# Kernel optimization log

Hardware: AMD Instinct MI355X
Metric: run time of the kernel (lower is better)

## Reference

```python
import jax, jax.numpy as jnp
import numpy as np


def setup_inputs() -> dict:
    key = jax.random.key(0)
    ks = jax.random.split(key, 6)
    B, S, F = 8, 2048, 1024
    scale = 1.0 / np.sqrt(F)
    return {
        "query": jax.random.normal(ks[0], (B, S, F), dtype=jnp.float32),
        "key": jax.random.normal(ks[1], (B, S, F), dtype=jnp.float32),
        "value": jax.random.normal(ks[2], (B, S, F), dtype=jnp.float32),
        "Wq": jax.random.normal(ks[3], (F, F), dtype=jnp.float32) * scale,
        "Wk": jax.random.normal(ks[4], (F, F), dtype=jnp.float32) * scale,
        "Wv": jax.random.normal(ks[5], (F, F), dtype=jnp.float32) * scale,
    }


def reference(query, key, value, Wq, Wk, Wv):
    # nn.Linear(bias=False): x @ W.T, W is [out, in]
    q_t = jnp.einsum('bsf,gf->bsg', query, Wq)
    k_t = jnp.einsum('bsf,gf->bsg', key, Wk)
    v_t = jnp.einsum('bsf,gf->bsg', value, Wv)
    F = k_t.shape[-1]
    scale = jnp.asarray(1.0, q_t.dtype) / jnp.sqrt(jnp.asarray(F, q_t.dtype))
    attn = jnp.einsum('bij,bkj->bik', q_t, k_t) * scale  # [B, S, S]
    # original uses nn.Softmax(dim=1): softmax over the query (i) axis
    attn = jax.nn.softmax(attn, axis=1)
    # 'bii,bij->bij': diagonal of attn scales rows of v_t
    diag = jnp.diagonal(attn, axis1=1, axis2=2)  # [B, S]
    proj = diag[:, :, None] * v_t  # [B, S, F]
    return proj
```

## Files before the change

### kernel.cpp

```cpp
#include <hip/hip_runtime.h>


typedef _Float16 f16x8 __attribute__((ext_vector_type(8)));
typedef float    f32x4 __attribute__((ext_vector_type(4)));

#define COLIC 8
#define SCALE 0.03125f

typedef __attribute__((address_space(1))) const unsigned int g_u32_t;
typedef __attribute__((address_space(3))) unsigned int l_u32_t;

__device__ __forceinline__ void gload16(const _Float16* g, _Float16* l) {
  __builtin_amdgcn_global_load_lds((g_u32_t*)g, (l_u32_t*)l, 16, 0, 0);
}

__device__ __forceinline__ void stage_tile(const _Float16* gbase, int ldk,
                                           _Float16* lds, int w, int lane) {
#pragma unroll
  for (int c = 0; c < 2; ++c) {
    const int blk = c * 4 + w;
    const int r = (blk << 4) + (lane >> 2);
    const _Float16* g = gbase + (size_t)r * ldk + ((lane & 3) << 3);
    gload16(g, lds + blk * 512);
  }
}

__device__ __forceinline__ void stage_tile64(const _Float16* gbase, int ldk,
                                             _Float16* lds, int w, int lane) {
#pragma unroll
  for (int c = 0; c < 4; ++c) {
    const int blk = c * 4 + w;
    const int o = (blk << 10) + (lane << 4);
    const int row = o >> 7;
    const int colb = (o & 127) ^ ((row & 7) << 4);
    gload16(gbase + (size_t)row * ldk + (colb >> 1), lds + (blk << 9));
  }
}

struct Conv3Args {
  const float* src[3];
  _Float16* dst[3];
};
__global__ __launch_bounds__(256)
void conv3_f32_f16(Conv3Args a, int n8) {
  const float* __restrict__ src = a.src[blockIdx.y];
  _Float16* __restrict__ dst = a.dst[blockIdx.y];
  for (int i = blockIdx.x * 256 + threadIdx.x; i < n8; i += gridDim.x * 256) {
    const float4 x = ((const float4*)src)[2 * i];
    const float4 y = ((const float4*)src)[2 * i + 1];
    f16x8 o;
    o[0] = (_Float16)x.x; o[1] = (_Float16)x.y;
    o[2] = (_Float16)x.z; o[3] = (_Float16)x.w;
    o[4] = (_Float16)y.x; o[5] = (_Float16)y.y;
    o[6] = (_Float16)y.z; o[7] = (_Float16)y.w;
    ((f16x8*)dst)[i] = o;
  }
}

template <int F16OUT>
__global__ __launch_bounds__(256)
void gemm_mfma(const float* __restrict__ Af, const _Float16* __restrict__ Bh,
               _Float16* __restrict__ C16, float* __restrict__ C32,
               const float* __restrict__ mpart, const float* __restrict__ lpart,
               const float* __restrict__ sdiag, int BSz,
               int M, int N, int Kd) {
  __shared__ __align__(16) _Float16 As[128 * 32];
  __shared__ __align__(16) _Float16 Bs[128 * 32];
  __shared__ float diagS[128];
  const int tid = threadIdx.x;
  const int w = tid >> 6, lane = tid & 63;
  const int wr = w >> 1, wc = w & 1;
  const int lr = lane & 15, kq = lane >> 4;
  const int bm = blockIdx.x * 128, bn = blockIdx.y * 128;

  if (!F16OUT && tid < 128) {
    const int row = bm + tid;
    float Mx = -3.0e38f;
#pragma unroll
    for (int c = 0; c < COLIC; ++c) Mx = fmaxf(Mx, mpart[(size_t)c * BSz + row]);
    float L = 0.0f;
#pragma unroll
    for (int c = 0; c < COLIC; ++c)
      L += lpart[(size_t)c * BSz + row] * __expf(mpart[(size_t)c * BSz + row] - Mx);
    diagS[tid] = __expf(sdiag[row] - Mx) / L;
  }

  const int ar = lane >> 2;
  const int ac = (lane & 3) << 3;
  float4 pa[2][2];
#pragma unroll
  for (int c = 0; c < 2; ++c) {
    const int row = bm + (c * 4 + w) * 16 + ar;
    const float4* p = (const float4*)(Af + (size_t)row * Kd + ac);
    pa[c][0] = p[0]; pa[c][1] = p[1];
  }

  f32x4 acc[4][4] = {};
  for (int k0 = 0; k0 < Kd; k0 += 32) {
#pragma unroll
    for (int c = 0; c < 2; ++c) {
      const int blk = c * 4 + w;
      f16x8 v;
      v[0] = (_Float16)pa[c][0].x; v[1] = (_Float16)pa[c][0].y;
      v[2] = (_Float16)pa[c][0].z; v[3] = (_Float16)pa[c][0].w;
      v[4] = (_Float16)pa[c][1].x; v[5] = (_Float16)pa[c][1].y;
      v[6] = (_Float16)pa[c][1].z; v[7] = (_Float16)pa[c][1].w;
      *(f16x8*)&As[blk * 512 + lane * 8] = v;
    }
    stage_tile(Bh + (size_t)bn * Kd + k0, Kd, Bs, w, lane);
    const int kn = (k0 + 32 < Kd) ? k0 + 32 : 0;
#pragma unroll
    for (int c = 0; c < 2; ++c) {
      const int row = bm + (c * 4 + w) * 16 + ar;
      const float4* p = (const float4*)(Af + (size_t)row * Kd + kn + ac);
      pa[c][0] = p[0]; pa[c][1] = p[1];
    }
    __syncthreads();
    f16x8 af[4], bf[4];
#pragma unroll
    for (int mi = 0; mi < 4; ++mi)
      af[mi] = *(const f16x8*)&As[(wr * 64 + mi * 16 + lr) * 32 + kq * 8];
#pragma unroll
    for (int ni = 0; ni < 4; ++ni)
      bf[ni] = *(const f16x8*)&Bs[(wc * 64 + ni * 16 + lr) * 32 + kq * 8];
#pragma unroll
    for (int mi = 0; mi < 4; ++mi)
#pragma unroll
      for (int ni = 0; ni < 4; ++ni)
        acc[mi][ni] = __builtin_amdgcn_mfma_f32_16x16x32_f16(af[mi], bf[ni], acc[mi][ni], 0, 0, 0);
    __syncthreads();
  }
#pragma unroll
  for (int mi = 0; mi < 4; ++mi) {
#pragma unroll
    for (int j = 0; j < 4; ++j) {
      const int rloc = wr * 64 + mi * 16 + kq * 4 + j;
      const int row = bm + rloc;
      float s = 1.0f;
      if (!F16OUT) s = diagS[rloc];
#pragma unroll
      for (int ni = 0; ni < 4; ++ni) {
        const int col = bn + wc * 64 + ni * 16 + lr;
        if (F16OUT) C16[(size_t)row * N + col] = (_Float16)acc[mi][ni][j];
        else        C32[(size_t)row * N + col] = acc[mi][ni][j] * s;
      }
    }
  }
}

__global__ __launch_bounds__(256)
void col_stats_mfma(const _Float16* __restrict__ qt, const _Float16* __restrict__ kt,
                    float* __restrict__ mpart, float* __restrict__ lpart,
                    float* __restrict__ sdiag, int S, int Fd, int chunk) {
  __shared__ __align__(16) _Float16 Qs[128 * 64];
  __shared__ __align__(16) _Float16 Ks[128 * 64];
  __shared__ float redM[8][128];
  __shared__ float redL[8][128];
  const int b = blockIdx.z, jb = blockIdx.x, ic = blockIdx.y;
  const int j0 = jb * 128;
  const _Float16* Q = qt + (size_t)b * S * Fd;
  const _Float16* K = kt + (size_t)b * S * Fd;
  const int tid = threadIdx.x;
  const int w = tid >> 6, lane = tid & 63;
  const int wr = w >> 1, wc = w & 1;
  const int lr = lane & 15, kq = lane >> 4;
  const int swz = (lr & 7) << 4;

  float m[4], l[4];
#pragma unroll
  for (int ni = 0; ni < 4; ++ni) { m[ni] = -3.0e38f; l[ni] = 0.0f; }

  for (int it = 0; it < chunk >> 7; ++it) {
    const int i0 = ic * chunk + (it << 7);
    f32x4 acc[4][4] = {};
    for (int k0 = 0; k0 < Fd; k0 += 64) {
      stage_tile64(Q + (size_t)i0 * Fd + k0, Fd, Qs, w, lane);
      stage_tile64(K + (size_t)j0 * Fd + k0, Fd, Ks, w, lane);
      __syncthreads();
      f16x8 af[4][2], bf[4][2];
#pragma unroll
      for (int mi = 0; mi < 4; ++mi) {
        const int ro = (wr * 64 + mi * 16 + lr) << 7;
        af[mi][0] = *(const f16x8*)&Qs[(ro + ((kq * 16) ^ swz)) >> 1];
        af[mi][1] = *(const f16x8*)&Qs[(ro + ((64 + kq * 16) ^ swz)) >> 1];
      }
#pragma unroll
      for (int ni = 0; ni < 4; ++ni) {
        const int ro = (wc * 64 + ni * 16 + lr) << 7;
        bf[ni][0] = *(const f16x8*)&Ks[(ro + ((kq * 16) ^ swz)) >> 1];
        bf[ni][1] = *(const f16x8*)&Ks[(ro + ((64 + kq * 16) ^ swz)) >> 1];
      }
#pragma unroll
      for (int ks = 0; ks < 2; ++ks)
#pragma unroll
        for (int mi = 0; mi < 4; ++mi)
#pragma unroll
          for (int ni = 0; ni < 4; ++ni)
            acc[mi][ni] = __builtin_amdgcn_mfma_f32_16x16x32_f16(af[mi][ks], bf[ni][ks], acc[mi][ni], 0, 0, 0);
      __syncthreads();
    }
    if (i0 == j0 && wr == wc && (lr >> 2) == kq) {
      const int j = lr & 3;
#pragma unroll
      for (int jj = 0; jj < 4; ++jj)
        sdiag[(size_t)b * S + j0 + wc * 64 + jj * 16 + lr] = acc[jj][jj][j] * SCALE;
    }
#pragma unroll
    for (int ni = 0; ni < 4; ++ni) {
      float tm = -3.0e38f;
#pragma unroll
      for (int mi = 0; mi < 4; ++mi)
#pragma unroll
        for (int jj = 0; jj < 4; ++jj) tm = fmaxf(tm, acc[mi][ni][jj]);
      tm *= SCALE;
      const float mn = fmaxf(m[ni], tm);
      float add = 0.0f;
#pragma unroll
      for (int mi = 0; mi < 4; ++mi)
#pragma unroll
        for (int jj = 0; jj < 4; ++jj) add += __expf(acc[mi][ni][jj] * SCALE - mn);
      l[ni] = l[ni] * __expf(m[ni] - mn) + add;
      m[ni] = mn;
    }
  }
  __syncthreads();
  const int p = wr * 4 + kq;
#pragma unroll
  for (int ni = 0; ni < 4; ++ni) {
    const int col = wc * 64 + ni * 16 + lr;
    redM[p][col] = m[ni];
    redL[p][col] = l[ni];
  }
  __syncthreads();
  if (tid < 128) {
    float M = -3.0e38f;
#pragma unroll
    for (int q = 0; q < 8; ++q) M = fmaxf(M, redM[q][tid]);
    float L = 0.0f;
#pragma unroll
    for (int q = 0; q < 8; ++q) L += redL[q][tid] * __expf(redM[q][tid] - M);
    const size_t idx = ((size_t)ic * gridDim.z + b) * S + j0 + tid;
    mpart[idx] = M;
    lpart[idx] = L;
  }
}

extern "C" void kernel_launch(void* const* d_in, const int* in_sizes, int n_in,
                              void* d_out, int out_size, void* d_ws, size_t ws_size,
                              hipStream_t stream) {
  const float* query = (const float*)d_in[0];
  const float* key   = (const float*)d_in[1];
  const float* value = (const float*)d_in[2];
  const float* Wq    = (const float*)d_in[3];
  const float* Wk    = (const float*)d_in[4];
  const float* Wv    = (const float*)d_in[5];

  const int F = 1024;
  const int BS = in_sizes[0] / F;
  const int B = 8;
  const int S = BS / B;

  _Float16* wq16 = (_Float16*)d_ws;
  _Float16* wk16 = wq16 + (size_t)F * F;
  _Float16* wv16 = wk16 + (size_t)F * F;
  float* mpart = (float*)(wv16 + (size_t)F * F);
  float* lpart = mpart + (size_t)COLIC * BS;
  float* sdiag = lpart + (size_t)COLIC * BS;

  _Float16* qt16 = (_Float16*)d_out;
  _Float16* kt16 = qt16 + (size_t)BS * F;

  const dim3 blk(256);
  const int n8w = F * F / 8;

  Conv3Args aw; aw.src[0] = Wq; aw.src[1] = Wk; aw.src[2] = Wv;
  aw.dst[0] = wq16; aw.dst[1] = wk16; aw.dst[2] = wv16;
  conv3_f32_f16<<<dim3(512, 3), blk, 0, stream>>>(aw, n8w);

  const dim3 ggrid(BS / 128, F / 128);
  gemm_mfma<1><<<ggrid, blk, 0, stream>>>(query, wq16, qt16, (float*)nullptr,
                                          (const float*)nullptr, (const float*)nullptr,
                                          (const float*)nullptr, BS, BS, F, F);
  gemm_mfma<1><<<ggrid, blk, 0, stream>>>(key, wk16, kt16, (float*)nullptr,
                                          (const float*)nullptr, (const float*)nullptr,
                                          (const float*)nullptr, BS, BS, F, F);

  const dim3 sgrid(S / 128, COLIC, B);
  col_stats_mfma<<<sgrid, blk, 0, stream>>>(qt16, kt16, mpart, lpart, sdiag,
                                            S, F, S / COLIC);

  gemm_mfma<0><<<ggrid, blk, 0, stream>>>(value, wv16, (_Float16*)nullptr, (float*)d_out,
                                          mpart, lpart, sdiag, BS, BS, F, F);
}
```

Measured before the change: 308.0 us.

## Pre-convert activations to fp16 and use async swizzled k64 staging in GEMMs

Adds a conversion pass that casts query, key and value to fp16 in workspace, so the projection GEMMs load fp16 A tiles via direct global-to-LDS loads instead of loading fp32 and converting in registers. The GEMM now stages 64-wide K tiles for both operands with an XOR-swizzled LDS layout to avoid bank conflicts and halve the number of barriers per K. This costs an extra full read/write pass over the activations and more workspace, in exchange for halved A-operand traffic per tile and a simpler, more efficient inner loop.

```diff
diff --git a/kernel.cpp b/kernel.cpp
--- a/kernel.cpp
+++ b/kernel.cpp
@@ -12,17 +12,6 @@
 
 __device__ __forceinline__ void gload16(const _Float16* g, _Float16* l) {
   __builtin_amdgcn_global_load_lds((g_u32_t*)g, (l_u32_t*)l, 16, 0, 0);
-}
-
-__device__ __forceinline__ void stage_tile(const _Float16* gbase, int ldk,
-                                           _Float16* lds, int w, int lane) {
-#pragma unroll
-  for (int c = 0; c < 2; ++c) {
-    const int blk = c * 4 + w;
-    const int r = (blk << 4) + (lane >> 2);
-    const _Float16* g = gbase + (size_t)r * ldk + ((lane & 3) << 3);
-    gload16(g, lds + blk * 512);
-  }
 }
 
 __device__ __forceinline__ void stage_tile64(const _Float16* gbase, int ldk,
@@ -59,18 +48,19 @@
 
 template <int F16OUT>
 __global__ __launch_bounds__(256)
-void gemm_mfma(const float* __restrict__ Af, const _Float16* __restrict__ Bh,
+void gemm_mfma(const _Float16* __restrict__ A, const _Float16* __restrict__ B,
                _Float16* __restrict__ C16, float* __restrict__ C32,
                const float* __restrict__ mpart, const float* __restrict__ lpart,
                const float* __restrict__ sdiag, int BSz,
                int M, int N, int Kd) {
-  __shared__ __align__(16) _Float16 As[128 * 32];
-  __shared__ __align__(16) _Float16 Bs[128 * 32];
+  __shared__ __align__(16) _Float16 As[128 * 64];
+  __shared__ __align__(16) _Float16 Bs[128 * 64];
   __shared__ float diagS[128];
   const int tid = threadIdx.x;
   const int w = tid >> 6, lane = tid & 63;
   const int wr = w >> 1, wc = w & 1;
   const int lr = lane & 15, kq = lane >> 4;
+  const int swz = (lr & 7) << 4;
   const int bm = blockIdx.x * 128, bn = blockIdx.y * 128;
 
   if (!F16OUT && tid < 128) {
@@ -85,49 +75,31 @@
     diagS[tid] = __expf(sdiag[row] - Mx) / L;
   }
 
-  const int ar = lane >> 2;
-  const int ac = (lane & 3) << 3;
-  float4 pa[2][2];
-#pragma unroll
-  for (int c = 0; c < 2; ++c) {
-    const int row = bm + (c * 4 + w) * 16 + ar;
-    const float4* p = (const float4*)(Af + (size_t)row * Kd + ac);
-    pa[c][0] = p[0]; pa[c][1] = p[1];
-  }
-
   f32x4 acc[4][4] = {};
-  for (int k0 = 0; k0 < Kd; k0 += 32) {
-#pragma unroll
-    for (int c = 0; c < 2; ++c) {
-      const int blk = c * 4 + w;
-      f16x8 v;
-      v[0] = (_Float16)pa[c][0].x; v[1] = (_Float16)pa[c][0].y;
-      v[2] = (_Float16)pa[c][0].z; v[3] = (_Float16)pa[c][0].w;
-      v[4] = (_Float16)pa[c][1].x; v[5] = (_Float16)pa[c][1].y;
-      v[6] = (_Float16)pa[c][1].z; v[7] = (_Float16)pa[c][1].w;
-      *(f16x8*)&As[blk * 512 + lane * 8] = v;
-    }
-    stage_tile(Bh + (size_t)bn * Kd + k0, Kd, Bs, w, lane);
-    const int kn = (k0 + 32 < Kd) ? k0 + 32 : 0;
-#pragma unroll
-    for (int c = 0; c < 2; ++c) {
-      const int row = bm + (c * 4 + w) * 16 + ar;
-      const float4* p = (const float4*)(Af + (size_t)row * Kd + kn + ac);
-      pa[c][0] = p[0]; pa[c][1] = p[1];
-    }
+  for (int k0 = 0; k0 < Kd; k0 += 64) {
+    stage_tile64(A + (size_t)bm * Kd + k0, Kd, As, w, lane);
+    stage_tile64(B + (size_t)bn * Kd + k0, Kd, Bs, w, lane);
     __syncthreads();
-    f16x8 af[4], bf[4];
-#pragma unroll
-    for (int mi = 0; mi < 4; ++mi)
-      af[mi] = *(const f16x8*)&As[(wr * 64 + mi * 16 + lr) * 32 + kq * 8];
-#pragma unroll
-    for (int ni = 0; ni < 4; ++ni)
-      bf[ni] = *(const f16x8*)&Bs[(wc * 64 + ni * 16 + lr) * 32 + kq * 8];
-#pragma unroll
-    for (int mi = 0; mi < 4; ++mi)
-#pragma unroll
-      for (int ni = 0; ni < 4; ++ni)
-        acc[mi][ni] = __builtin_amdgcn_mfma_f32_16x16x32_f16(af[mi], bf[ni], acc[mi][ni], 0, 0, 0);
+    f16x8 af[4][2], bf[4][2];
+#pragma unroll
+    for (int mi = 0; mi < 4; ++mi) {
+      const int ro = (wr * 64 + mi * 16 + lr) << 7;
+      af[mi][0] = *(const f16x8*)&As[(ro + ((kq * 16) ^ swz)) >> 1];
+      af[mi][1] = *(const f16x8*)&As[(ro + ((64 + kq * 16) ^ swz)) >> 1];
+    }
+#pragma unroll
+    for (int ni = 0; ni < 4; ++ni) {
+      const int ro = (wc * 64 + ni * 16 + lr) << 7;
+      bf[ni][0] = *(const f16x8*)&Bs[(ro + ((kq * 16) ^ swz)) >> 1];
+      bf[ni][1] = *(const f16x8*)&Bs[(ro + ((64 + kq * 16) ^ swz)) >> 1];
+    }
+#pragma unroll
+    for (int ks = 0; ks < 2; ++ks)
+#pragma unroll
+      for (int mi = 0; mi < 4; ++mi)
+#pragma unroll
+        for (int ni = 0; ni < 4; ++ni)
+          acc[mi][ni] = __builtin_amdgcn_mfma_f32_16x16x32_f16(af[mi][ks], bf[ni][ks], acc[mi][ni], 0, 0, 0);
     __syncthreads();
   }
 #pragma unroll
@@ -260,7 +232,10 @@
   const int B = 8;
   const int S = BS / B;
 
-  _Float16* wq16 = (_Float16*)d_ws;
+  _Float16* q16  = (_Float16*)d_ws;
+  _Float16* k16  = q16 + (size_t)BS * F;
+  _Float16* v16  = k16 + (size_t)BS * F;
+  _Float16* wq16 = v16 + (size_t)BS * F;
   _Float16* wk16 = wq16 + (size_t)F * F;
   _Float16* wv16 = wk16 + (size_t)F * F;
   float* mpart = (float*)(wv16 + (size_t)F * F);
@@ -271,17 +246,21 @@
   _Float16* kt16 = qt16 + (size_t)BS * F;
 
   const dim3 blk(256);
-  const int n8w = F * F / 8;
+  const int n8x = BS * F / 8, n8w = F * F / 8;
+
+  Conv3Args ax; ax.src[0] = query; ax.src[1] = key; ax.src[2] = value;
+  ax.dst[0] = q16; ax.dst[1] = k16; ax.dst[2] = v16;
+  conv3_f32_f16<<<dim3(2048, 3), blk, 0, stream>>>(ax, n8x);
 
   Conv3Args aw; aw.src[0] = Wq; aw.src[1] = Wk; aw.src[2] = Wv;
   aw.dst[0] = wq16; aw.dst[1] = wk16; aw.dst[2] = wv16;
   conv3_f32_f16<<<dim3(512, 3), blk, 0, stream>>>(aw, n8w);
 
   const dim3 ggrid(BS / 128, F / 128);
-  gemm_mfma<1><<<ggrid, blk, 0, stream>>>(query, wq16, qt16, (float*)nullptr,
+  gemm_mfma<1><<<ggrid, blk, 0, stream>>>(q16, wq16, qt16, (float*)nullptr,
                                           (const float*)nullptr, (const float*)nullptr,
                                           (const float*)nullptr, BS, BS, F, F);
-  gemm_mfma<1><<<ggrid, blk, 0, stream>>>(key, wk16, kt16, (float*)nullptr,
+  gemm_mfma<1><<<ggrid, blk, 0, stream>>>(k16, wk16, kt16, (float*)nullptr,
                                           (const float*)nullptr, (const float*)nullptr,
                                           (const float*)nullptr, BS, BS, F, F);
 
@@ -289,6 +268,6 @@
   col_stats_mfma<<<sgrid, blk, 0, stream>>>(qt16, kt16, mpart, lpart, sdiag,
                                             S, F, S / COLIC);
 
-  gemm_mfma<0><<<ggrid, blk, 0, stream>>>(value, wv16, (_Float16*)nullptr, (float*)d_out,
+  gemm_mfma<0><<<ggrid, blk, 0, stream>>>(v16, wv16, (_Float16*)nullptr, (float*)d_out,
                                           mpart, lpart, sdiag, BS, BS, F, F);
 }
```

Result: faster. 281.8 us (-8.5%).
